# Performance work log

Measured on AMD Instinct MI355X. Metric: run time of the kernel, lower is better.

The kernel has to match this reference:

```python
import jax, jax.numpy as jnp
import numpy as np

D_MODEL = 1024
N_HEADS = 16
D_HEAD = D_MODEL // N_HEADS
B, T = 4, 2048


def setup_inputs() -> dict:
    key = jax.random.key(0)
    ks = jax.random.split(key, 9)
    s = 0.02
    return {
        "x": jax.random.normal(ks[0], (B, T, D_MODEL), dtype=jnp.float32),
        "Wq": jax.random.normal(ks[1], (D_MODEL, D_MODEL), dtype=jnp.float32) * s,
        "bq": jnp.zeros((D_MODEL,), dtype=jnp.float32),
        "Wk": jax.random.normal(ks[2], (D_MODEL, D_MODEL), dtype=jnp.float32) * s,
        "bk": jnp.zeros((D_MODEL,), dtype=jnp.float32),
        "Wv": jax.random.normal(ks[3], (D_MODEL, D_MODEL), dtype=jnp.float32) * s,
        "bv": jnp.zeros((D_MODEL,), dtype=jnp.float32),
        "Wo": jax.random.normal(ks[4], (D_MODEL, D_MODEL), dtype=jnp.float32) * s,
        "bo": jnp.zeros((D_MODEL,), dtype=jnp.float32),
    }


def reference(x, Wq, bq, Wk, bk, Wv, bv, Wo, bo):
    # Dropout in eval mode (identity), as standard for a correctness baseline.
    Bx, Tx, _ = x.shape
    # torch nn.Linear: y = x @ W.T + b
    Q = x @ Wq.T + bq
    K = x @ Wk.T + bk
    V = x @ Wv.T + bv
    # [B, T, H, Dh] -> [B, H, T, Dh]
    Q = Q.reshape(Bx, Tx, N_HEADS, D_HEAD).transpose(0, 2, 1, 3)
    K = K.reshape(Bx, Tx, N_HEADS, D_HEAD).transpose(0, 2, 1, 3)
    V = V.reshape(Bx, Tx, N_HEADS, D_HEAD).transpose(0, 2, 1, 3)
    scale = 1.0 / jnp.sqrt(jnp.float32(D_HEAD))
    scores = jnp.einsum("bhqd,bhkd->bhqk", Q, K) * scale  # [B,H,T,T]
    # additive causal mask: -1e6 above the diagonal (matches torch.triu trick)
    mask = jnp.triu(jnp.full((Tx, Tx), -1000000.0, dtype=scores.dtype), k=1)
    scores = scores + mask
    attn = jax.nn.softmax(scores, axis=-1)
    out = jnp.einsum("bhqk,bhkd->bhqd", attn, V)  # [B,H,T,Dh]
    out = out.transpose(0, 2, 1, 3).reshape(Bx, Tx, D_MODEL)
    out = out @ Wo.T + bo
    return out
```

## Files before the change

### kernel.cpp

```cpp
#include <hip/hip_runtime.h>
#include <stdint.h>

#define DM 1024
#define HEADS 16
#define DH 64
#define BQ 4
#define TT 2048
#define MTOT (BQ*TT)
#define NQT (TT/64)

typedef __attribute__((ext_vector_type(8))) __bf16 bf16x8;
typedef __attribute__((ext_vector_type(4))) float f32x4;
typedef __attribute__((ext_vector_type(4))) uint32_t u32x4;
typedef unsigned short u16;
typedef __attribute__((ext_vector_type(8))) unsigned short u16x8;

__device__ __forceinline__ u16 f2b(float f) {
  uint32_t u = __builtin_bit_cast(uint32_t, f);
  u = (u + 0x7fffu + ((u >> 16) & 1u)) >> 16;
  return (u16)u;
}

__device__ __forceinline__ uint32_t cvtpk(float lo, float hi) {
  uint32_t r;
  asm("v_cvt_pk_bf16_f32 %0, %1, %2" : "=v"(r) : "v"(lo), "v"(hi));
  return r;
}

__device__ __forceinline__ void gload_lds16(const u16* g, u16* l) {
  __builtin_amdgcn_global_load_lds(
      (const __attribute__((address_space(1))) void*)g,
      (__attribute__((address_space(3))) void*)l, 16, 0, 0);
}

#define NX (MTOT * DM / 4)
#define NW (DM * DM / 4)
__global__ __launch_bounds__(256) void cast_all(const float* __restrict__ x,
                                                const float* __restrict__ Wq,
                                                const float* __restrict__ Wk,
                                                const float* __restrict__ Wv,
                                                const float* __restrict__ Wo,
                                                u16* __restrict__ xb,
                                                u16* __restrict__ wqkvb,
                                                u16* __restrict__ wob) {
  int i = blockIdx.x * 256 + threadIdx.x;
  const float* src; u16* dst;
  if (i < NX)               { src = x;  dst = xb; }
  else if (i < NX + NW)     { src = Wq; dst = wqkvb;          i -= NX; }
  else if (i < NX + 2 * NW) { src = Wk; dst = wqkvb + 4 * NW; i -= NX + NW; }
  else if (i < NX + 3 * NW) { src = Wv; dst = wqkvb + 8 * NW; i -= NX + 2 * NW; }
  else                      { src = Wo; dst = wob;            i -= NX + 3 * NW; }
  float4 v = ((const float4*)src)[i];
  ushort4 o;
  o.x = f2b(v.x); o.y = f2b(v.y); o.z = f2b(v.z); o.w = f2b(v.w);
  ((ushort4*)dst)[i] = o;
}

#define NK2 16
#define SLOT_A2 (256 * 64)
#define SLOT_B2 (128 * 64)
#define SLOT_E2 (SLOT_A2 + SLOT_B2)

__global__ __launch_bounds__(512, 2) void gemm_qkv8(const u16* __restrict__ A,
                                                    const u16* __restrict__ W,
                                                    const float* __restrict__ bq,
                                                    const float* __restrict__ bk,
                                                    const float* __restrict__ bv,
                                                    u16* __restrict__ Qo,
                                                    u16* __restrict__ Ko,
                                                    u16* __restrict__ Vto,
                                                    float qs) {
  __shared__ u16 lds[3 * SLOT_E2];
  const int tid = threadIdx.x, lane = tid & 63, wave = tid >> 6;
  const int fr = lane & 15, g = lane >> 4;
  const int wm = wave >> 1, wn = wave & 1;

  int bid = blockIdx.x;
  bid = (bid & 7) * 96 + (bid >> 3);
  const int by = bid / 24, bx = bid % 24;
  const int m0 = by * 256, n0 = bx * 128;

  const int lr8 = lane >> 3;
  const int lsc = ((lane & 7) ^ lr8) * 8;
  const u16* gA0 = A + (size_t)(m0 + wave * 8 + lr8) * DM + lsc;
  const u16* gB0 = W + (size_t)(n0 + wave * 8 + lr8) * DM + lsc;
  const int dA0 = wave * 512;
  const int dB0 = SLOT_A2 + wave * 512;

#define STAGEQ(ls, kt) {                                     \
    const int ke = (kt) * 64;                                \
    gload_lds16(gA0 + ke,                (ls) + dA0);        \
    gload_lds16(gA0 + ke + (size_t)64  * DM, (ls) + dA0 + 4096);  \
    gload_lds16(gA0 + ke + (size_t)128 * DM, (ls) + dA0 + 8192);  \
    gload_lds16(gA0 + ke + (size_t)192 * DM, (ls) + dA0 + 12288); \
    gload_lds16(gB0 + ke,                (ls) + dB0);        \
    gload_lds16(gB0 + ke + (size_t)64  * DM, (ls) + dB0 + 4096); }

  const int rc0 = ((g) ^ (fr & 7)) * 8;
  const int rc1 = ((4 + g) ^ (fr & 7)) * 8;
  const int offA = (wm * 64 + fr) * 64;
  const int offB = SLOT_A2 + (wn * 64 + fr) * 64;

  f32x4 acc[4][4];
#pragma unroll
  for (int mi = 0; mi < 4; ++mi)
#pragma unroll
    for (int ni = 0; ni < 4; ++ni) acc[mi][ni] = (f32x4){0.f, 0.f, 0.f, 0.f};

  bf16x8 afA[8], bfA[8], afB[8], bfB[8];

#define READQ(AFv, BFv, ls) {                                \
    _Pragma("unroll")                                        \
    for (int mi = 0; mi < 4; ++mi) {                         \
      AFv[2 * mi]     = *(const bf16x8*)&(ls)[offA + mi * 1024 + rc0]; \
      AFv[2 * mi + 1] = *(const bf16x8*)&(ls)[offA + mi * 1024 + rc1]; \
    }                                                        \
    _Pragma("unroll")                                        \
    for (int ni = 0; ni < 4; ++ni) {                         \
      BFv[2 * ni]     = *(const bf16x8*)&(ls)[offB + ni * 1024 + rc0]; \
      BFv[2 * ni + 1] = *(const bf16x8*)&(ls)[offB + ni * 1024 + rc1]; \
    } }

#define MFMAQ(AFv, BFv) {                                    \
    __builtin_amdgcn_s_setprio(1);                           \
    _Pragma("unroll")                                        \
    for (int mi = 0; mi < 4; ++mi)                           \
      _Pragma("unroll")                                      \
      for (int ni = 0; ni < 4; ++ni) {                       \
        acc[mi][ni] = __builtin_amdgcn_mfma_f32_16x16x32_bf16(AFv[2 * mi], BFv[2 * ni], acc[mi][ni], 0, 0, 0); \
        acc[mi][ni] = __builtin_amdgcn_mfma_f32_16x16x32_bf16(AFv[2 * mi + 1], BFv[2 * ni + 1], acc[mi][ni], 0, 0, 0); \
      }                                                      \
    __builtin_amdgcn_s_setprio(0); }

#define QW6 asm volatile("s_waitcnt vmcnt(6)" ::: "memory"); \
            asm volatile("s_barrier" ::: "memory");
#define QW0 asm volatile("s_waitcnt vmcnt(0)" ::: "memory"); \
            asm volatile("s_barrier" ::: "memory");

  u16* p0 = &lds[0];
  u16* p1 = &lds[SLOT_E2];
  u16* p2 = &lds[2 * SLOT_E2];
  u16 *pCur = p0, *pNxt = p1, *pStg = p2;

  STAGEQ(p0, 0)
  STAGEQ(p1, 1)
  asm volatile("s_waitcnt vmcnt(6)" ::: "memory");
  asm volatile("s_barrier" ::: "memory");
  READQ(afA, bfA, p0)

  for (int kt = 0; kt < NK2 - 2; kt += 2) {
    STAGEQ(pStg, kt + 2)
    QW6
    READQ(afB, bfB, pNxt)
    MFMAQ(afA, bfA)
    { u16* t = pCur; pCur = pNxt; pNxt = pStg; pStg = t; }
    if (kt + 3 < NK2) { STAGEQ(pStg, kt + 3) }
    QW6
    READQ(afA, bfA, pNxt)
    MFMAQ(afB, bfB)
    { u16* t = pCur; pCur = pNxt; pNxt = pStg; pStg = t; }
  }
  QW0
  READQ(afB, bfB, pNxt)
  MFMAQ(afA, bfA)
  MFMAQ(afB, bfB)

  const int g4 = g * 4;
  const int seg = n0 >> 10;
  const int nbase = (n0 & 1023) + wn * 64 + fr;
  if (seg == 0) {
#pragma unroll
    for (int ni = 0; ni < 4; ++ni) {
      const int cgl = nbase + ni * 16;
      const float bb = bq[cgl];
      const int hh = cgl >> 6, d = cgl & 63;
#pragma unroll
      for (int mi = 0; mi < 4; ++mi) {
        const int m = m0 + wm * 64 + mi * 16 + g4;
        const int bi = m >> 11, t = m & 2047;
        u16* dst = &Qo[(((size_t)bi * HEADS + hh) * TT + t) * DH + d];
#pragma unroll
        for (int j = 0; j < 4; ++j)
          dst[(size_t)j * DH] = f2b((acc[mi][ni][j] + bb) * qs);
      }
    }
  } else if (seg == 1) {
#pragma unroll
    for (int ni = 0; ni < 4; ++ni) {
      const int cgl = nbase + ni * 16;
      const float bb = bk[cgl];
      const int hh = cgl >> 6, d = cgl & 63;
#pragma unroll
      for (int mi = 0; mi < 4; ++mi) {
        const int m = m0 + wm * 64 + mi * 16 + g4;
        const int bi = m >> 11, t = m & 2047;
        u16* dst = &Ko[(((size_t)bi * HEADS + hh) * TT + t) * DH + d];
#pragma unroll
        for (int j = 0; j < 4; ++j)
          dst[(size_t)j * DH] = f2b(acc[mi][ni][j] + bb);
      }
    }
  } else {
#pragma unroll
    for (int ni = 0; ni < 4; ++ni) {
      const int cgl = nbase + ni * 16;
      const float bb = bv[cgl];
      const int hh = cgl >> 6, d = cgl & 63;
#pragma unroll
      for (int mi = 0; mi < 4; ++mi) {
        const int m = m0 + wm * 64 + mi * 16 + g4;
        const int t0 = m & 2047, bi = m >> 11;
        const int w64 = t0 & 63;
        const int pos = (t0 & ~63) | (((w64 >> 5) & 1) << 5) | (((w64 >> 2) & 3) << 3) |
                        (((w64 >> 4) & 1) << 2);
        ushort4 o;
        o.x = f2b(acc[mi][ni][0] + bb);
        o.y = f2b(acc[mi][ni][1] + bb);
        o.z = f2b(acc[mi][ni][2] + bb);
        o.w = f2b(acc[mi][ni][3] + bb);
        *(ushort4*)&Vto[(((size_t)bi * HEADS + hh) * DH + d) * TT + pos] = o;
      }
    }
  }
#undef STAGEQ
#undef READQ
#undef MFMAQ
#undef QW6
#undef QW0
}

#define SLOT_OA (256 * 32)
#define SLOT_OB (128 * 32)
#define SLOT_OE (SLOT_OA + SLOT_OB)

__global__ __launch_bounds__(512, 2) void gemm_out8(const u16* __restrict__ A,
                                                    const u16* __restrict__ Bw,
                                                    const float* __restrict__ bias,
                                                    float* __restrict__ outp) {
  __shared__ u16 lds[4 * SLOT_OE];
  const int tid = threadIdx.x, lane = tid & 63, wave = tid >> 6;
  const int fr = lane & 15, g = lane >> 4;
  const int wm = wave >> 1, wn = wave & 1;

  const int bx = blockIdx.x >> 5, by = blockIdx.x & 31;
  const int m0 = by * 256, n0 = bx * 128;

  const int srow = tid >> 2;
  const int schunk = (tid & 3) ^ ((tid >> 3) & 3);
  const u16* gA0 = A + (size_t)(m0 + srow) * DM + schunk * 8;
  const u16* gA1 = gA0 + (size_t)128 * DM;
  const u16* gB0 = Bw + (size_t)(n0 + srow) * DM + schunk * 8;
  const int dA0 = wave * 512;
  const int dA1 = 4096 + wave * 512;
  const int dB0 = SLOT_OA + wave * 512;

#define STAGEO(slot, kt) {                                   \
    u16* ls = &lds[(slot) * SLOT_OE];                        \
    const int ke = (kt) * 32;                                \
    gload_lds16(gA0 + ke, ls + dA0);                         \
    gload_lds16(gA1 + ke, ls + dA1);                         \
    gload_lds16(gB0 + ke, ls + dB0); }

  const int rchunk = (g ^ ((fr >> 1) & 3)) * 8;
  const int offA = (wm * 64 + fr) * 32 + rchunk;
  const int offB = SLOT_OA + (wn * 64 + fr) * 32 + rchunk;

  f32x4 acc[4][4];
#pragma unroll
  for (int mi = 0; mi < 4; ++mi)
#pragma unroll
    for (int ni = 0; ni < 4; ++ni) acc[mi][ni] = (f32x4){0.f, 0.f, 0.f, 0.f};

  bf16x8 afA[4], bfA[4], afB[4], bfB[4];

#define READO(AFv, BFv, kt) {                                \
    const u16* sl = &lds[((kt) & 3) * SLOT_OE];              \
    _Pragma("unroll")                                        \
    for (int mi = 0; mi < 4; ++mi)                           \
      AFv[mi] = *(const bf16x8*)&sl[offA + mi * 512];        \
    _Pragma("unroll")                                        \
    for (int ni = 0; ni < 4; ++ni)                           \
      BFv[ni] = *(const bf16x8*)&sl[offB + ni * 512]; }

#define MFMAO(AFv, BFv) {                                    \
    __builtin_amdgcn_s_setprio(1);                           \
    _Pragma("unroll")                                        \
    for (int mi = 0; mi < 4; ++mi)                           \
      _Pragma("unroll")                                      \
      for (int ni = 0; ni < 4; ++ni)                         \
        acc[mi][ni] = __builtin_amdgcn_mfma_f32_16x16x32_bf16(AFv[mi], BFv[ni], acc[mi][ni], 0, 0, 0); \
    __builtin_amdgcn_s_setprio(0); }

#define OW3 asm volatile("s_waitcnt vmcnt(3)" ::: "memory"); \
            asm volatile("s_barrier" ::: "memory");
#define OW0 asm volatile("s_waitcnt vmcnt(0)" ::: "memory"); \
            asm volatile("s_barrier" ::: "memory");

  STAGEO(0, 0)
  STAGEO(1, 1)
  STAGEO(2, 2)
  asm volatile("s_waitcnt vmcnt(6)" ::: "memory");
  asm volatile("s_barrier" ::: "memory");
  READO(afA, bfA, 0)

  for (int kt = 0; kt < 28; kt += 2) {
    OW3
    READO(afB, bfB, kt + 1)
    MFMAO(afA, bfA)
    STAGEO((kt + 3) & 3, kt + 3)
    OW3
    READO(afA, bfA, kt + 2)
    MFMAO(afB, bfB)
    STAGEO((kt + 4) & 3, kt + 4)
  }
  OW3
  READO(afB, bfB, 29)
  MFMAO(afA, bfA)
  STAGEO(3, 31)
  OW3
  READO(afA, bfA, 30)
  MFMAO(afB, bfB)
  OW0
  READO(afB, bfB, 31)
  MFMAO(afA, bfA)
  MFMAO(afB, bfB)

  const int g4 = g * 4;
#pragma unroll
  for (int mi = 0; mi < 4; ++mi) {
    const int rg = m0 + wm * 64 + mi * 16 + g4;
#pragma unroll
    for (int ni = 0; ni < 4; ++ni) {
      const int cg = n0 + wn * 64 + ni * 16 + fr;
      const float bb = bias[cg];
#pragma unroll
      for (int j = 0; j < 4; ++j)
        outp[(size_t)(rg + j) * DM + cg] = acc[mi][ni][j] + bb;
    }
  }
#undef STAGEO
#undef READO
#undef MFMAO
#undef OW3
#undef OW0
}

__global__ __launch_bounds__(256) void attn_fwd(const u16* __restrict__ Q,
                                                const u16* __restrict__ K,
                                                const u16* __restrict__ Vt,
                                                u16* __restrict__ O) {
  const int o_ = blockIdx.x;
  const int xcd = o_ & 7, j = o_ >> 3;
  const int gi = j & 7;
  const int qt128 = 15 - (j >> 3);
  const int gidx = xcd * 8 + gi;
  const int b = gidx >> 4, h = gidx & 15;
  const int tid = threadIdx.x, lane = tid & 63, wave = tid >> 6;
  __shared__ u16 Ks[2][64 * 64];
  __shared__ u16 Vs[2][64 * 64];

  const size_t bh = ((size_t)b * HEADS + h) * TT;
  const size_t vbse = ((size_t)b * HEADS + h) * DH;
  const int fr = lane & 15, g = lane >> 4;

  const int srow = wave * 16 + (lane & 15);
  const int gp = lane >> 4;
  const int wc0 = (gp ^ (srow & 7)) * 8;
  const int wc1 = ((gp + 4) ^ (srow & 7)) * 8;
  const int ldw = srow * 64;
  const u16* kRow = &K[(bh + srow) * DH + gp * 8];
  const u16* vRow = &Vt[(vbse + srow) * TT + gp * 8];

  const int rk0 = (g ^ (fr & 7)) * 8;
  const int rk1 = ((4 + g) ^ (fr & 7)) * 8;
  const int k8 = g * 8;

  const int q0 = qt128 * 128;
  const int qtL = 2 * qt128, qtH = qtL + 1;
  const int qrowL = q0 + wave * 16 + fr;
  const int qrowH = q0 + 64 + wave * 16 + fr;
  const bf16x8 qfL0 = *(const bf16x8*)&Q[(bh + qrowL) * DH + k8];
  const bf16x8 qfL1 = *(const bf16x8*)&Q[(bh + qrowL) * DH + 32 + k8];
  const bf16x8 qfH0 = *(const bf16x8*)&Q[(bh + qrowH) * DH + k8];
  const bf16x8 qfH1 = *(const bf16x8*)&Q[(bh + qrowH) * DH + 32 + k8];

  float lsumL = 0.f, lsumH = 0.f;
  f32x4 oaccL[4], oaccH[4];
#pragma unroll
  for (int c = 0; c < 4; ++c) {
    oaccL[c] = (f32x4){0.f, 0.f, 0.f, 0.f};
    oaccH[c] = (f32x4){0.f, 0.f, 0.f, 0.f};
  }

#define LOADKV(KA, KC, VA, VC, kv0) {                       \
    KA = *(const u16x8*)(kRow + (size_t)(kv0) * DH);        \
    KC = *(const u16x8*)(kRow + (size_t)(kv0) * DH + 32);   \
    VA = *(const u16x8*)(vRow + (kv0));                     \
    VC = *(const u16x8*)(vRow + (kv0) + 32); }

#define WRITEKV(BUF, KA, KC, VA, VC) {                      \
    *(u16x8*)&Ks[BUF][ldw + wc0] = KA;                      \
    *(u16x8*)&Ks[BUF][ldw + wc1] = KC;                      \
    *(u16x8*)&Vs[BUF][ldw + wc0] = VA;                      \
    *(u16x8*)&Vs[BUF][ldw + wc1] = VC; }

#define COMPUTE_T(BUF, kvb) {                                                  \
    f32x4 sL[4], sH[4];                                                        \
    __builtin_amdgcn_s_setprio(1);                                             \
    _Pragma("unroll")                                                          \
    for (int c = 0; c < 4; ++c) {                                              \
      bf16x8 kb0 = *(const bf16x8*)&Ks[BUF][(c * 16 + fr) * 64 + rk0];         \
      bf16x8 kb1 = *(const bf16x8*)&Ks[BUF][(c * 16 + fr) * 64 + rk1];         \
      f32x4 tL = (f32x4){0.f, 0.f, 0.f, 0.f};                                  \
      tL = __builtin_amdgcn_mfma_f32_16x16x32_bf16(kb0, qfL0, tL, 0, 0, 0);    \
      tL = __builtin_amdgcn_mfma_f32_16x16x32_bf16(kb1, qfL1, tL, 0, 0, 0);    \
      sL[c] = tL;                                                              \
      f32x4 tH = (f32x4){0.f, 0.f, 0.f, 0.f};                                  \
      tH = __builtin_amdgcn_mfma_f32_16x16x32_bf16(kb0, qfH0, tH, 0, 0, 0);    \
      tH = __builtin_amdgcn_mfma_f32_16x16x32_bf16(kb1, qfH1, tH, 0, 0, 0);    \
      sH[c] = tH;                                                              \
    }                                                                          \
    __builtin_amdgcn_s_setprio(0);                                             \
    if ((kvb) >= qtL) {                                                        \
      const int kvm = (kvb) * 64;                                              \
      _Pragma("unroll")                                                        \
      for (int c = 0; c < 4; ++c) {                                            \
        const int colg = kvm + c * 16 + 4 * g;                                 \
        _Pragma("unroll")                                                      \
        for (int r = 0; r < 4; ++r) {                                          \
          if (colg + r > qrowL) sL[c][r] = -1e30f;                             \
          if (colg + r > qrowH) sH[c][r] = -1e30f;                             \
        }                                                                      \
      }                                                                        \
    }                                                                          \
    float rsL = 0.f, rsH = 0.f;                                                \
    uint32_t pkL[8], pkH[8];                                                   \
    _Pragma("unroll")                                                          \
    for (int c = 0; c < 4; ++c) {                                              \
      float l0 = __builtin_amdgcn_exp2f(sL[c][0]);                             \
      float l1 = __builtin_amdgcn_exp2f(sL[c][1]);                             \
      float l2 = __builtin_amdgcn_exp2f(sL[c][2]);                             \
      float l3 = __builtin_amdgcn_exp2f(sL[c][3]);                             \
      rsL += (l0 + l1) + (l2 + l3);                                            \
      pkL[2 * c] = cvtpk(l0, l1);                                              \
      pkL[2 * c + 1] = cvtpk(l2, l3);                                          \
      float h0 = __builtin_amdgcn_exp2f(sH[c][0]);                             \
      float h1 = __builtin_amdgcn_exp2f(sH[c][1]);                             \
      float h2 = __builtin_amdgcn_exp2f(sH[c][2]);                             \
      float h3 = __builtin_amdgcn_exp2f(sH[c][3]);                             \
      rsH += (h0 + h1) + (h2 + h3);                                            \
      pkH[2 * c] = cvtpk(h0, h1);                                              \
      pkH[2 * c + 1] = cvtpk(h2, h3);                                          \
    }                                                                          \
    rsL += __shfl_xor(rsL, 16);                                                \
    rsL += __shfl_xor(rsL, 32);                                                \
    lsumL += rsL;                                                              \
    rsH += __shfl_xor(rsH, 16);                                                \
    rsH += __shfl_xor(rsH, 32);                                                \
    lsumH += rsH;                                                              \
    const bf16x8 paL0 = __builtin_bit_cast(bf16x8, (u32x4){pkL[0], pkL[1], pkL[2], pkL[3]}); \
    const bf16x8 paL1 = __builtin_bit_cast(bf16x8, (u32x4){pkL[4], pkL[5], pkL[6], pkL[7]}); \
    const bf16x8 paH0 = __builtin_bit_cast(bf16x8, (u32x4){pkH[0], pkH[1], pkH[2], pkH[3]}); \
    const bf16x8 paH1 = __builtin_bit_cast(bf16x8, (u32x4){pkH[4], pkH[5], pkH[6], pkH[7]}); \
    __builtin_amdgcn_s_setprio(1);                                             \
    _Pragma("unroll")                                                          \
    for (int c = 0; c < 4; ++c) {                                              \
      bf16x8 vb0 = *(const bf16x8*)&Vs[BUF][(c * 16 + fr) * 64 + rk0];         \
      bf16x8 vb1 = *(const bf16x8*)&Vs[BUF][(c * 16 + fr) * 64 + rk1];         \
      oaccL[c] = __builtin_amdgcn_mfma_f32_16x16x32_bf16(vb0, paL0, oaccL[c], 0, 0, 0); \
      oaccL[c] = __builtin_amdgcn_mfma_f32_16x16x32_bf16(vb1, paL1, oaccL[c], 0, 0, 0); \
      oaccH[c] = __builtin_amdgcn_mfma_f32_16x16x32_bf16(vb0, paH0, oaccH[c], 0, 0, 0); \
      oaccH[c] = __builtin_amdgcn_mfma_f32_16x16x32_bf16(vb1, paH1, oaccH[c], 0, 0, 0); \
    }                                                                          \
    __builtin_amdgcn_s_setprio(0);                                             \
  }

  u16x8 kaA, kcA, vaA, vcA, kaB, kcB, vaB, vcB;
  LOADKV(kaA, kcA, vaA, vcA, 0)

  for (int it = 0; it <= qt128; ++it) {
    const int kvA = 2 * it, kvB = 2 * it + 1;
    WRITEKV(0, kaA, kcA, vaA, vcA)
    LOADKV(kaB, kcB, vaB, vcB, kvB * 64)
    __syncthreads();
    COMPUTE_T(0, kvA)
    WRITEKV(1, kaB, kcB, vaB, vcB)
    if (it < qt128) LOADKV(kaA, kcA, vaA, vcA, (kvB + 1) * 64)
    __syncthreads();
    COMPUTE_T(1, kvB)
  }

  const float invL = 1.f / lsumL;
#pragma unroll
  for (int c = 0; c < 4; ++c) {
    ushort4 o;
    o.x = f2b(oaccL[c][0] * invL);
    o.y = f2b(oaccL[c][1] * invL);
    o.z = f2b(oaccL[c][2] * invL);
    o.w = f2b(oaccL[c][3] * invL);
    *(ushort4*)&O[((size_t)b * TT + qrowL) * DM + h * DH + c * 16 + 4 * g] = o;
  }
  const float invH = 1.f / lsumH;
#pragma unroll
  for (int c = 0; c < 4; ++c) {
    ushort4 o;
    o.x = f2b(oaccH[c][0] * invH);
    o.y = f2b(oaccH[c][1] * invH);
    o.z = f2b(oaccH[c][2] * invH);
    o.w = f2b(oaccH[c][3] * invH);
    *(ushort4*)&O[((size_t)b * TT + qrowH) * DM + h * DH + c * 16 + 4 * g] = o;
  }
#undef LOADKV
#undef WRITEKV
#undef COMPUTE_T
}

extern "C" void kernel_launch(void* const* d_in, const int* in_sizes, int n_in,
                              void* d_out, int out_size, void* d_ws, size_t ws_size,
                              hipStream_t stream) {
  const float* x  = (const float*)d_in[0];
  const float* Wq = (const float*)d_in[1];
  const float* bq = (const float*)d_in[2];
  const float* Wk = (const float*)d_in[3];
  const float* bk = (const float*)d_in[4];
  const float* Wv = (const float*)d_in[5];
  const float* bv = (const float*)d_in[6];
  const float* Wo = (const float*)d_in[7];
  const float* bo = (const float*)d_in[8];

  char* w = (char*)d_ws;
  u16* xb    = (u16*)w; w += (size_t)MTOT * DM * 2;
  u16* Wqkvb = (u16*)w; w += (size_t)3 * DM * DM * 2;
  u16* Wob   = (u16*)w; w += (size_t)DM * DM * 2;
  u16* Qb    = (u16*)w; w += (size_t)MTOT * DM * 2;
  u16* Kb    = (u16*)w; w += (size_t)MTOT * DM * 2;
  u16* Vtb   = (u16*)w; w += (size_t)MTOT * DM * 2;
  u16* AOb   = (u16*)w; w += (size_t)MTOT * DM * 2;

  cast_all<<<(NX + 4 * NW) / 256, 256, 0, stream>>>(x, Wq, Wk, Wv, Wo, xb, Wqkvb, Wob);

  const float qs = 0.125f * 1.44269504f;
  gemm_qkv8<<<768, 512, 0, stream>>>(xb, Wqkvb, bq, bk, bv, Qb, Kb, Vtb, qs);

  attn_fwd<<<1024, 256, 0, stream>>>(Qb, Kb, Vtb, AOb);

  gemm_out8<<<256, 512, 0, stream>>>(AOb, Wob, bo, (float*)d_out);
}
```

Measured before the change: 161.5 us.

## Stage 128-key KV tiles per sync instead of double-buffered 64-key tiles

Replaces the two-buffer 64-row K/V ping-pong with a single 128-row shared tile. Each thread now writes its slice of both halves, one barrier follows, the next tile's global loads are issued, and two 64-key halves are computed before a closing barrier. This halves the loop iterations but keeps two barriers per 128 keys, so the number of barriers is unchanged. It also removes the overlap between writing one LDS buffer and computing on the other, and it doubles the registers held for prefetched K/V.

```diff
diff --git a/kernel.cpp b/kernel.cpp
--- a/kernel.cpp
+++ b/kernel.cpp
@@ -356,24 +356,24 @@
   const int gidx = xcd * 8 + gi;
   const int b = gidx >> 4, h = gidx & 15;
   const int tid = threadIdx.x, lane = tid & 63, wave = tid >> 6;
-  __shared__ u16 Ks[2][64 * 64];
-  __shared__ u16 Vs[2][64 * 64];
+  __shared__ u16 Ks[128 * 64];
+  __shared__ u16 Vs[128 * 64];
 
   const size_t bh = ((size_t)b * HEADS + h) * TT;
   const size_t vbse = ((size_t)b * HEADS + h) * DH;
   const int fr = lane & 15, g = lane >> 4;
-
-  const int srow = wave * 16 + (lane & 15);
-  const int gp = lane >> 4;
-  const int wc0 = (gp ^ (srow & 7)) * 8;
-  const int wc1 = ((gp + 4) ^ (srow & 7)) * 8;
-  const int ldw = srow * 64;
-  const u16* kRow = &K[(bh + srow) * DH + gp * 8];
-  const u16* vRow = &Vt[(vbse + srow) * TT + gp * 8];
-
+  const int sr = tid >> 2;
+  const int sc0 = tid & 3;
+
+  const int sw1 = (sc0 ^ (sr & 7)) * 8;
+  const int sw2 = ((sc0 + 4) ^ (sr & 7)) * 8;
+  const int sgc = sc0 * 8;
   const int rk0 = (g ^ (fr & 7)) * 8;
   const int rk1 = ((4 + g) ^ (fr & 7)) * 8;
   const int k8 = g * 8;
+
+  const u16* kBase = &K[(bh + sr) * DH + sgc];
+  const u16* vBase = &Vt[(vbse + sr) * TT + sgc];
 
   const int q0 = qt128 * 128;
   const int qtL = 2 * qt128, qtH = qtL + 1;
@@ -392,25 +392,25 @@
     oaccH[c] = (f32x4){0.f, 0.f, 0.f, 0.f};
   }
 
-#define LOADKV(KA, KC, VA, VC, kv0) {                       \
-    KA = *(const u16x8*)(kRow + (size_t)(kv0) * DH);        \
-    KC = *(const u16x8*)(kRow + (size_t)(kv0) * DH + 32);   \
-    VA = *(const u16x8*)(vRow + (kv0));                     \
-    VC = *(const u16x8*)(vRow + (kv0) + 32); }
-
-#define WRITEKV(BUF, KA, KC, VA, VC) {                      \
-    *(u16x8*)&Ks[BUF][ldw + wc0] = KA;                      \
-    *(u16x8*)&Ks[BUF][ldw + wc1] = KC;                      \
-    *(u16x8*)&Vs[BUF][ldw + wc0] = VA;                      \
-    *(u16x8*)&Vs[BUF][ldw + wc1] = VC; }
-
-#define COMPUTE_T(BUF, kvb) {                                                  \
+  u16x8 k0a, k0c, v0a, v0c, k1a, k1c, v1a, v1c;
+#define LOADH0(kv0) {                                        \
+    k0a = *(const u16x8*)(kBase + (size_t)(kv0) * DH);       \
+    k0c = *(const u16x8*)(kBase + (size_t)(kv0) * DH + 32);  \
+    v0a = *(const u16x8*)(vBase + (kv0));                    \
+    v0c = *(const u16x8*)(vBase + (kv0) + 32); }
+#define LOADH1(kv0) {                                        \
+    k1a = *(const u16x8*)(kBase + (size_t)((kv0) + 64) * DH);      \
+    k1c = *(const u16x8*)(kBase + (size_t)((kv0) + 64) * DH + 32); \
+    v1a = *(const u16x8*)(vBase + (kv0) + 64);               \
+    v1c = *(const u16x8*)(vBase + (kv0) + 96); }
+
+#define COMPUTE_H(RO, kvt) {                                                   \
     f32x4 sL[4], sH[4];                                                        \
     __builtin_amdgcn_s_setprio(1);                                             \
     _Pragma("unroll")                                                          \
     for (int c = 0; c < 4; ++c) {                                              \
-      bf16x8 kb0 = *(const bf16x8*)&Ks[BUF][(c * 16 + fr) * 64 + rk0];         \
-      bf16x8 kb1 = *(const bf16x8*)&Ks[BUF][(c * 16 + fr) * 64 + rk1];         \
+      bf16x8 kb0 = *(const bf16x8*)&Ks[((RO) + c * 16 + fr) * 64 + rk0];       \
+      bf16x8 kb1 = *(const bf16x8*)&Ks[((RO) + c * 16 + fr) * 64 + rk1];       \
       f32x4 tL = (f32x4){0.f, 0.f, 0.f, 0.f};                                  \
       tL = __builtin_amdgcn_mfma_f32_16x16x32_bf16(kb0, qfL0, tL, 0, 0, 0);    \
       tL = __builtin_amdgcn_mfma_f32_16x16x32_bf16(kb1, qfL1, tL, 0, 0, 0);    \
@@ -421,8 +421,8 @@
       sH[c] = tH;                                                              \
     }                                                                          \
     __builtin_amdgcn_s_setprio(0);                                             \
-    if ((kvb) >= qtL) {                                                        \
-      const int kvm = (kvb) * 64;                                              \
+    if ((kvt) >= qtL) {                                                        \
+      const int kvm = (kvt) * 64;                                              \
       _Pragma("unroll")                                                        \
       for (int c = 0; c < 4; ++c) {                                            \
         const int colg = kvm + c * 16 + 4 * g;                                 \
@@ -465,8 +465,8 @@
     __builtin_amdgcn_s_setprio(1);                                             \
     _Pragma("unroll")                                                          \
     for (int c = 0; c < 4; ++c) {                                              \
-      bf16x8 vb0 = *(const bf16x8*)&Vs[BUF][(c * 16 + fr) * 64 + rk0];         \
-      bf16x8 vb1 = *(const bf16x8*)&Vs[BUF][(c * 16 + fr) * 64 + rk1];         \
+      bf16x8 vb0 = *(const bf16x8*)&Vs[((RO) + c * 16 + fr) * 64 + rk0];       \
+      bf16x8 vb1 = *(const bf16x8*)&Vs[((RO) + c * 16 + fr) * 64 + rk1];       \
       oaccL[c] = __builtin_amdgcn_mfma_f32_16x16x32_bf16(vb0, paL0, oaccL[c], 0, 0, 0); \
       oaccL[c] = __builtin_amdgcn_mfma_f32_16x16x32_bf16(vb1, paL1, oaccL[c], 0, 0, 0); \
       oaccH[c] = __builtin_amdgcn_mfma_f32_16x16x32_bf16(vb0, paH0, oaccH[c], 0, 0, 0); \
@@ -475,19 +475,29 @@
     __builtin_amdgcn_s_setprio(0);                                             \
   }
 
-  u16x8 kaA, kcA, vaA, vcA, kaB, kcB, vaB, vcB;
-  LOADKV(kaA, kcA, vaA, vcA, 0)
+  LOADH0(0)
+  LOADH1(0)
 
   for (int it = 0; it <= qt128; ++it) {
-    const int kvA = 2 * it, kvB = 2 * it + 1;
-    WRITEKV(0, kaA, kcA, vaA, vcA)
-    LOADKV(kaB, kcB, vaB, vcB, kvB * 64)
+    *(u16x8*)&Ks[sr * 64 + sw1] = k0a;
+    *(u16x8*)&Ks[sr * 64 + sw2] = k0c;
+    *(u16x8*)&Vs[sr * 64 + sw1] = v0a;
+    *(u16x8*)&Vs[sr * 64 + sw2] = v0c;
+    *(u16x8*)&Ks[(64 + sr) * 64 + sw1] = k1a;
+    *(u16x8*)&Ks[(64 + sr) * 64 + sw2] = k1c;
+    *(u16x8*)&Vs[(64 + sr) * 64 + sw1] = v1a;
+    *(u16x8*)&Vs[(64 + sr) * 64 + sw2] = v1c;
     __syncthreads();
-    COMPUTE_T(0, kvA)
-    WRITEKV(1, kaB, kcB, vaB, vcB)
-    if (it < qt128) LOADKV(kaA, kcA, vaA, vcA, (kvB + 1) * 64)
+
+    if (it < qt128) {
+      const int nkv = (it + 1) * 128;
+      LOADH0(nkv)
+      LOADH1(nkv)
+    }
+
+    COMPUTE_H(0, 2 * it)
+    COMPUTE_H(64, 2 * it + 1)
     __syncthreads();
-    COMPUTE_T(1, kvB)
   }
 
   const float invL = 1.f / lsumL;
@@ -510,9 +520,9 @@
     o.w = f2b(oaccH[c][3] * invH);
     *(ushort4*)&O[((size_t)b * TT + qrowH) * DM + h * DH + c * 16 + 4 * g] = o;
   }
-#undef LOADKV
-#undef WRITEKV
-#undef COMPUTE_T
+#undef LOADH0
+#undef LOADH1
+#undef COMPUTE_H
 }
 
 extern "C" void kernel_launch(void* const* d_in, const int* in_sizes, int n_in,
```

After: 161.7 us. About the same (+0.1%).
